# Optimization experiments

Measured on AMD Instinct MI355X. Metric: run time of the kernel, lower is better.

## Reference

```python
import jax, jax.numpy as jnp
import numpy as np

N_AGENTS = 8
N_ACTIONS = 14
STATE_DIM = 168
RNN_DIM = 64
GAT_DIM = 32
N_HEADS = 4
HYPER = 64


def setup_inputs() -> dict:
    key = jax.random.key(0)
    ks = jax.random.split(key, 16)
    bs, T = 256, 256
    def xavier(k, shape):
        fan_in, fan_out = shape[0], shape[-1]
        lim = float(np.sqrt(6.0 / (fan_in + fan_out)))
        return jax.random.uniform(k, shape, jnp.float32, -lim, lim)
    return {
        'agent_qs': jax.random.normal(ks[0], (bs, T, N_AGENTS), jnp.float32),
        'states': jax.random.normal(ks[1], (bs, T, STATE_DIM), jnp.float32),
        'max_q_i': jax.random.normal(ks[2], (bs, T, N_AGENTS), jnp.float32),
        'hidden_states': jax.random.normal(ks[3], (bs, T, N_AGENTS, RNN_DIM), jnp.float32),
        # hyper_w_final MLP
        'w1f': xavier(ks[4], (STATE_DIM, HYPER)), 'b1f': jnp.zeros((HYPER,), jnp.float32),
        'w2f': xavier(ks[5], (HYPER, N_AGENTS)), 'b2f': jnp.zeros((N_AGENTS,), jnp.float32),
        # V MLP
        'w1v': xavier(ks[6], (STATE_DIM, HYPER)), 'b1v': jnp.zeros((HYPER,), jnp.float32),
        'w2v': xavier(ks[7], (HYPER, N_AGENTS)), 'b2v': jnp.zeros((N_AGENTS,), jnp.float32),
        # GAT: W (no bias) and attention vector att_a [1, H, 2*d]
        'Wg': xavier(ks[8], (RNN_DIM, N_HEADS * GAT_DIM)),
        'att_a': xavier(ks[9], (1, N_HEADS, 2 * GAT_DIM)) * 1.414,
        # hyper_w_dvd linear
        'Wd': xavier(ks[10], (STATE_DIM, N_HEADS * GAT_DIM)), 'bd': jnp.zeros((N_HEADS * GAT_DIM,), jnp.float32),
    }


def reference(agent_qs, states, max_q_i, hidden_states,
              w1f, b1f, w2f, b2f, w1v, b1v, w2v, b2v,
              Wg, att_a, Wd, bd):
    bs = agent_qs.shape[0]
    S = states.reshape(-1, STATE_DIM)                     # [B, state_dim]
    q = agent_qs.reshape(-1, N_AGENTS)                    # [B, n]
    mq = max_q_i.reshape(-1, N_AGENTS)
    H = hidden_states.reshape(-1, N_AGENTS, RNN_DIM)      # [B, n, rnn]

    # weighted_head=True branch
    w_final = jnp.abs(jax.nn.relu(S @ w1f + b1f) @ w2f + b2f) + 1e-10
    v = jax.nn.relu(S @ w1v + b1v) @ w2v + b2v
    q = w_final * q + v
    mq = w_final * mq + v
    adv_q = jax.lax.stop_gradient(q - mq)                 # .detach() in torch

    # MultiHeadGAT on tiny agent graph, without materializing h_cat
    hp = jnp.einsum('bni,ihd->bhnd', H, Wg.reshape(RNN_DIM, N_HEADS, GAT_DIM))  # [B,h,n,d]
    a_i = att_a[0, :, :GAT_DIM]                           # [h, d]
    a_j = att_a[0, :, GAT_DIM:]
    e_i = jnp.einsum('bhnd,hd->bhn', hp, a_i)
    e_j = jnp.einsum('bhnd,hd->bhn', hp, a_j)
    e = e_i[:, :, :, None] + e_j[:, :, None, :]           # [B,h,n,n]
    e = jnp.where(e > 0, e, 0.2 * e)                      # LeakyReLU(0.2)
    attn = jax.nn.softmax(e, axis=-1)
    graphs = jax.nn.elu(jnp.einsum('bhij,bhjd->bhid', attn, hp))  # [B,h,n,d]

    # DVD weights
    w_dvd = (S @ Wd + bd).reshape(-1, N_HEADS, GAT_DIM)   # [B,h,d]
    weights_dvd = jnp.abs(jnp.einsum('bhd,bhnd->bhn', w_dvd, graphs))  # [B,h,n]
    adv_w_final = weights_dvd.mean(axis=1)                # [B,n]

    # is_minus_one=True
    adv_tot = jnp.sum(adv_q * (adv_w_final - 1.0), axis=1)
    return adv_tot.reshape(bs, -1, 1)
```

## Files before the change

### kernel.cpp

```cpp
#include <hip/hip_runtime.h>
#include <math.h>

#define STATE_DIM 168
#define BTOT 65536
#define SLS 1064

typedef float f32x4 __attribute__((ext_vector_type(4)));
typedef short bf16x8 __attribute__((ext_vector_type(8)));

union Frag { bf16x8 v; unsigned short u[8]; };
union Acc  { f32x4 v; float f[4]; };

__device__ __forceinline__ unsigned short f2bf(float f) {
    unsigned int u = __float_as_uint(f);
    u += 0x7fffu + ((u >> 16) & 1u);
    return (unsigned short)(u >> 16);
}

__global__ void __launch_bounds__(256, 5)
ffn_kernel(const float* __restrict__ states,
           const float* __restrict__ w1f, const float* __restrict__ b1f,
           const float* __restrict__ w2f, const float* __restrict__ b2f,
           const float* __restrict__ Wd,  const float* __restrict__ bd,
           float* __restrict__ wfin, float* __restrict__ wdvd)
{
    __shared__ float S_lds[4][8 * STATE_DIM];
    __shared__ float y1_lds[4][8 * 65];

    const int wid  = threadIdx.x >> 6;
    const int lane = threadIdx.x & 63;
    const int wgi  = blockIdx.x * 4 + wid;
    const long s0  = (long)wgi * 8;

    const float* Sg = states + s0 * STATE_DIM;
    float* Sl = S_lds[wid];
    #pragma unroll
    for (int i = 0; i < 21; ++i)
        Sl[lane + i * 64] = Sg[lane + i * 64];
    __syncthreads();

    float acc1[8], ad0[8], ad1[8];
    const float bb1  = b1f[lane];
    const float bdv0 = bd[lane];
    const float bdv1 = bd[lane + 64];
    #pragma unroll
    for (int s = 0; s < 8; ++s) { acc1[s] = bb1; ad0[s] = bdv0; ad1[s] = bdv1; }

    float w1c[4], wd0c[4], wd1c[4];
    #pragma unroll
    for (int kk = 0; kk < 4; ++kk) {
        w1c[kk]  = w1f[kk * 64 + lane];
        wd0c[kk] = Wd[kk * 128 + lane];
        wd1c[kk] = Wd[kk * 128 + 64 + lane];
    }

    for (int k = 0; k < STATE_DIM; k += 4) {
        const int kn = (k + 4 < STATE_DIM) ? (k + 4) : k;
        float w1n[4], wd0n[4], wd1n[4];
        #pragma unroll
        for (int kk = 0; kk < 4; ++kk) {
            w1n[kk]  = w1f[(kn + kk) * 64 + lane];
            wd0n[kk] = Wd[(kn + kk) * 128 + lane];
            wd1n[kk] = Wd[(kn + kk) * 128 + 64 + lane];
        }
        #pragma unroll
        for (int s = 0; s < 8; ++s) {
            const float4 sv = *(const float4*)&Sl[s * STATE_DIM + k];
            acc1[s] = fmaf(sv.x, w1c[0], acc1[s]);
            acc1[s] = fmaf(sv.y, w1c[1], acc1[s]);
            acc1[s] = fmaf(sv.z, w1c[2], acc1[s]);
            acc1[s] = fmaf(sv.w, w1c[3], acc1[s]);
            ad0[s] = fmaf(sv.x, wd0c[0], ad0[s]);
            ad0[s] = fmaf(sv.y, wd0c[1], ad0[s]);
            ad0[s] = fmaf(sv.z, wd0c[2], ad0[s]);
            ad0[s] = fmaf(sv.w, wd0c[3], ad0[s]);
            ad1[s] = fmaf(sv.x, wd1c[0], ad1[s]);
            ad1[s] = fmaf(sv.y, wd1c[1], ad1[s]);
            ad1[s] = fmaf(sv.z, wd1c[2], ad1[s]);
            ad1[s] = fmaf(sv.w, wd1c[3], ad1[s]);
        }
        #pragma unroll
        for (int kk = 0; kk < 4; ++kk) {
            w1c[kk] = w1n[kk]; wd0c[kk] = wd0n[kk]; wd1c[kk] = wd1n[kk];
        }
    }

    #pragma unroll
    for (int s = 0; s < 8; ++s) {
        y1_lds[wid][s * 65 + lane] = fmaxf(acc1[s], 0.0f);
        wdvd[(s0 + s) * 128 + lane]      = ad0[s];
        wdvd[(s0 + s) * 128 + 64 + lane] = ad1[s];
    }
    __syncthreads();

    {
        const int s = lane >> 3, n = lane & 7;
        float acc = b2f[n];
        #pragma unroll
        for (int j = 0; j < 64; ++j)
            acc = fmaf(y1_lds[wid][s * 65 + j], w2f[j * 8 + n], acc);
        wfin[(s0 + s) * 8 + n] = fabsf(acc) + 1e-10f;
    }
}

__global__ void __launch_bounds__(256, 3)
gat_kernel(const float* __restrict__ agent_qs,
           const float* __restrict__ max_q_i,
           const float* __restrict__ hidden,
           const float* __restrict__ Wg,
           const float* __restrict__ att_a,
           const float* __restrict__ wfin,
           const float* __restrict__ wdvd,
           float* __restrict__ out)
{
    __shared__ float hp_lds[4][2 * SLS];
    __shared__ float attn_lds[4][544];
    __shared__ float e_lds[4][128];
    __shared__ float ws_lds[4][64];
    __shared__ float a_lds[264];

    const int t    = threadIdx.x;
    const int wid  = t >> 6;
    const int lane = t & 63;

    {
        const int h = t >> 6, r = t & 63, wch = r >> 5, d = r & 31;
        a_lds[(h * 2 + wch) * 33 + d] = att_a[t];
    }
    __syncthreads();

    float* hp  = hp_lds[wid];
    float* at  = attn_lds[wid];
    float* el  = e_lds[wid];
    float* wsl = ws_lds[wid];

    const int wgid = blockIdx.x * 4 + wid;
    const int quad = lane >> 4;
    const int col  = lane & 15;

    Frag Bf[8][2];
    #pragma unroll
    for (int tt = 0; tt < 8; ++tt)
        #pragma unroll
        for (int ks = 0; ks < 2; ++ks)
            #pragma unroll
            for (int j = 0; j < 8; ++j)
                Bf[tt][ks].u[j] =
                    f2bf(Wg[(ks * 32 + quad * 8 + j) * 128 + tt * 16 + col]);

    const int sl_a = (lane >> 3) & 1;
    const int n_a  = lane & 7;
    const int sl_w = quad >> 1;
    const int nb   = (quad & 1) * 4;

    for (int g = 0; g < 4; ++g) {
        const long smp0 = (long)wgid * 8 + 2 * g;

        Frag A0, A1;
        {
            const float* Hb = hidden + (smp0 + sl_a) * 512 + n_a * 64 + quad * 8;
            const float4 h00 = *(const float4*)(Hb);
            const float4 h01 = *(const float4*)(Hb + 4);
            const float4 h10 = *(const float4*)(Hb + 32);
            const float4 h11 = *(const float4*)(Hb + 36);
            A0.u[0] = f2bf(h00.x); A0.u[1] = f2bf(h00.y);
            A0.u[2] = f2bf(h00.z); A0.u[3] = f2bf(h00.w);
            A0.u[4] = f2bf(h01.x); A0.u[5] = f2bf(h01.y);
            A0.u[6] = f2bf(h01.z); A0.u[7] = f2bf(h01.w);
            A1.u[0] = f2bf(h10.x); A1.u[1] = f2bf(h10.y);
            A1.u[2] = f2bf(h10.z); A1.u[3] = f2bf(h10.w);
            A1.u[4] = f2bf(h11.x); A1.u[5] = f2bf(h11.y);
            A1.u[6] = f2bf(h11.z); A1.u[7] = f2bf(h11.w);
        }

        #pragma unroll
        for (int tt = 0; tt < 8; ++tt) {
            Acc acc;
            acc.v = (f32x4){0.f, 0.f, 0.f, 0.f};
            acc.v = __builtin_amdgcn_mfma_f32_16x16x32_bf16(A0.v, Bf[tt][0].v, acc.v, 0, 0, 0);
            acc.v = __builtin_amdgcn_mfma_f32_16x16x32_bf16(A1.v, Bf[tt][1].v, acc.v, 0, 0, 0);
            const int c = tt * 16 + col;
            float4 st = {acc.f[0], acc.f[1], acc.f[2], acc.f[3]};
            *(float4*)&hp[sl_w * SLS + c * 8 + ((c >> 5) << 3) + nb] = st;
        }

        {
            const int h = lane >> 4, r = lane & 15, wch = r >> 3, n = r & 7;
            const float* arow = &a_lds[(h * 2 + wch) * 33];
            #pragma unroll
            for (int sl = 0; sl < 2; ++sl) {
                float acc = 0.f;
                #pragma unroll
                for (int d = 0; d < 32; ++d)
                    acc = fmaf(hp[sl * SLS + (h * 32 + d) * 8 + h * 8 + n],
                               arow[d], acc);
                el[sl * 64 + wch * 32 + h * 8 + n] = acc;
            }
        }

        {
            const int sl = lane >> 5, r = lane & 31, h = r >> 3, i = r & 7;
            const float eiv = el[sl * 64 + h * 8 + i];
            const float* ejp = &el[sl * 64 + 32 + h * 8];
            float e[8], mx = -1e30f;
            #pragma unroll
            for (int j = 0; j < 8; ++j) {
                float v = eiv + ejp[j];
                v = v > 0.f ? v : 0.2f * v;
                e[j] = v;
                mx = fmaxf(mx, v);
            }
            float ssum = 0.f;
            #pragma unroll
            for (int j = 0; j < 8; ++j) { e[j] = __expf(e[j] - mx); ssum += e[j]; }
            const float inv = 1.f / ssum;
            #pragma unroll
            for (int j = 0; j < 8; ++j)
                at[sl * 272 + h * 66 + i * 8 + j] = e[j] * inv;
        }

        {
            const int sl = lane >> 5, r = lane & 31, h = r >> 3, n = r & 7;
            const long smp = smp0 + sl;
            float ar[8];
            #pragma unroll
            for (int j = 0; j < 8; ++j)
                ar[j] = at[sl * 272 + h * 66 + n * 8 + j];
            float wdd[32];
            {
                const float* wdp = wdvd + smp * 128 + h * 32;
                #pragma unroll
                for (int q4 = 0; q4 < 8; ++q4) {
                    const float4 v = *(const float4*)(wdp + q4 * 4);
                    wdd[q4 * 4 + 0] = v.x; wdd[q4 * 4 + 1] = v.y;
                    wdd[q4 * 4 + 2] = v.z; wdd[q4 * 4 + 3] = v.w;
                }
            }
            float part = 0.f;
            #pragma unroll
            for (int d = 0; d < 32; ++d) {
                const int c = h * 32 + d;
                const float* hb = &hp[sl * SLS + c * 8 + h * 8];
                const float4 p0 = *(const float4*)(hb);
                const float4 p1 = *(const float4*)(hb + 4);
                float gg = ar[0] * p0.x;
                gg = fmaf(ar[1], p0.y, gg);
                gg = fmaf(ar[2], p0.z, gg);
                gg = fmaf(ar[3], p0.w, gg);
                gg = fmaf(ar[4], p1.x, gg);
                gg = fmaf(ar[5], p1.y, gg);
                gg = fmaf(ar[6], p1.z, gg);
                gg = fmaf(ar[7], p1.w, gg);
                gg = gg > 0.f ? gg : (__expf(gg) - 1.0f);
                part = fmaf(wdd[d], gg, part);
            }
            wsl[sl * 32 + h * 8 + n] = fabsf(part);
        }

        {
            const int sl = lane >> 5, r = lane & 31;
            if (r < 8) {
                const int n = r;
                const long smp = smp0 + sl;
                const float awf = 0.25f * (wsl[sl * 32 + n] + wsl[sl * 32 + 8 + n] +
                                           wsl[sl * 32 + 16 + n] + wsl[sl * 32 + 24 + n]);
                const float adv = wfin[smp * 8 + n] *
                                  (agent_qs[smp * 8 + n] - max_q_i[smp * 8 + n]);
                float p = adv * (awf - 1.0f);
                p += __shfl_xor(p, 4, 64);
                p += __shfl_xor(p, 2, 64);
                p += __shfl_xor(p, 1, 64);
                if (n == 0) out[smp] = p;
            }
        }
    }
}

extern "C" void kernel_launch(void* const* d_in, const int* in_sizes, int n_in,
                              void* d_out, int out_size, void* d_ws, size_t ws_size,
                              hipStream_t stream) {
    const float* agent_qs = (const float*)d_in[0];
    const float* states   = (const float*)d_in[1];
    const float* max_q_i  = (const float*)d_in[2];
    const float* hidden   = (const float*)d_in[3];
    const float* w1f = (const float*)d_in[4];
    const float* b1f = (const float*)d_in[5];
    const float* w2f = (const float*)d_in[6];
    const float* b2f = (const float*)d_in[7];
    const float* Wg    = (const float*)d_in[12];
    const float* att_a = (const float*)d_in[13];
    const float* Wd    = (const float*)d_in[14];
    const float* bd    = (const float*)d_in[15];
    float* out  = (float*)d_out;

    float* wfin = (float*)d_ws;
    float* wdvd = wfin + (size_t)BTOT * 8;

    ffn_kernel<<<2048, 256, 0, stream>>>(states, w1f, b1f, w2f, b2f, Wd, bd,
                                         wfin, wdvd);
    gat_kernel<<<2048, 256, 0, stream>>>(agent_qs, max_q_i, hidden, Wg, att_a,
                                         wfin, wdvd, out);
}
```

Measured before the change: 364.3 us.

## Rewrite state FFN kernel with bf16 MFMA and register-resident weight fragments

Replaces the scalar FP32 FMA loop of the FFN kernel with bf16 16x16x32 MFMA instructions. Weight fragments for w1f, Wd and w2f are converted to bf16 and held in registers once per block, while each block processes two 16-sample tiles staged through padded bf16 LDS. The intent is to cut the ALU cost of the 168-wide projections. It lowers precision to bf16 for the states and weights, and it leaves the separate GAT kernel unchanged.

```diff
diff --git a/kernel.cpp b/kernel.cpp
--- a/kernel.cpp
+++ b/kernel.cpp
@@ -4,6 +4,7 @@
 #define STATE_DIM 168
 #define BTOT 65536
 #define SLS 1064
+#define SPAD 184
 
 typedef float f32x4 __attribute__((ext_vector_type(4)));
 typedef short bf16x8 __attribute__((ext_vector_type(8)));
@@ -17,89 +18,116 @@
     return (unsigned short)(u >> 16);
 }
 
-__global__ void __launch_bounds__(256, 5)
+__global__ void __launch_bounds__(256)
 ffn_kernel(const float* __restrict__ states,
            const float* __restrict__ w1f, const float* __restrict__ b1f,
            const float* __restrict__ w2f, const float* __restrict__ b2f,
            const float* __restrict__ Wd,  const float* __restrict__ bd,
            float* __restrict__ wfin, float* __restrict__ wdvd)
 {
-    __shared__ float S_lds[4][8 * STATE_DIM];
-    __shared__ float y1_lds[4][8 * 65];
-
-    const int wid  = threadIdx.x >> 6;
-    const int lane = threadIdx.x & 63;
-    const int wgi  = blockIdx.x * 4 + wid;
-    const long s0  = (long)wgi * 8;
-
-    const float* Sg = states + s0 * STATE_DIM;
-    float* Sl = S_lds[wid];
+    __shared__ unsigned short S_bf[16 * SPAD];
+    __shared__ float y1[16 * 72];
+
+    const int t    = threadIdx.x;
+    const int wid  = t >> 6;
+    const int lane = t & 63;
+    const int quad = lane >> 4;
+    const int col  = lane & 15;
+
+    Frag B[3][6];
     #pragma unroll
-    for (int i = 0; i < 21; ++i)
-        Sl[lane + i * 64] = Sg[lane + i * 64];
-    __syncthreads();
-
-    float acc1[8], ad0[8], ad1[8];
-    const float bb1  = b1f[lane];
-    const float bdv0 = bd[lane];
-    const float bdv1 = bd[lane + 64];
+    for (int ks = 0; ks < 6; ++ks)
+        #pragma unroll
+        for (int j = 0; j < 8; ++j) {
+            const int k = ks * 32 + quad * 8 + j;
+            const bool v = (k < STATE_DIM);
+            B[0][ks].u[j] = v ? f2bf(w1f[k * 64 + wid * 16 + col]) : (unsigned short)0;
+            B[1][ks].u[j] = v ? f2bf(Wd[k * 128 + wid * 32 + col]) : (unsigned short)0;
+            B[2][ks].u[j] = v ? f2bf(Wd[k * 128 + wid * 32 + 16 + col]) : (unsigned short)0;
+        }
+    Frag B2[2];
     #pragma unroll
-    for (int s = 0; s < 8; ++s) { acc1[s] = bb1; ad0[s] = bdv0; ad1[s] = bdv1; }
-
-    float w1c[4], wd0c[4], wd1c[4];
-    #pragma unroll
-    for (int kk = 0; kk < 4; ++kk) {
-        w1c[kk]  = w1f[kk * 64 + lane];
-        wd0c[kk] = Wd[kk * 128 + lane];
-        wd1c[kk] = Wd[kk * 128 + 64 + lane];
-    }
-
-    for (int k = 0; k < STATE_DIM; k += 4) {
-        const int kn = (k + 4 < STATE_DIM) ? (k + 4) : k;
-        float w1n[4], wd0n[4], wd1n[4];
-        #pragma unroll
-        for (int kk = 0; kk < 4; ++kk) {
-            w1n[kk]  = w1f[(kn + kk) * 64 + lane];
-            wd0n[kk] = Wd[(kn + kk) * 128 + lane];
-            wd1n[kk] = Wd[(kn + kk) * 128 + 64 + lane];
-        }
-        #pragma unroll
-        for (int s = 0; s < 8; ++s) {
-            const float4 sv = *(const float4*)&Sl[s * STATE_DIM + k];
-            acc1[s] = fmaf(sv.x, w1c[0], acc1[s]);
-            acc1[s] = fmaf(sv.y, w1c[1], acc1[s]);
-            acc1[s] = fmaf(sv.z, w1c[2], acc1[s]);
-            acc1[s] = fmaf(sv.w, w1c[3], acc1[s]);
-            ad0[s] = fmaf(sv.x, wd0c[0], ad0[s]);
-            ad0[s] = fmaf(sv.y, wd0c[1], ad0[s]);
-            ad0[s] = fmaf(sv.z, wd0c[2], ad0[s]);
-            ad0[s] = fmaf(sv.w, wd0c[3], ad0[s]);
-            ad1[s] = fmaf(sv.x, wd1c[0], ad1[s]);
-            ad1[s] = fmaf(sv.y, wd1c[1], ad1[s]);
-            ad1[s] = fmaf(sv.z, wd1c[2], ad1[s]);
-            ad1[s] = fmaf(sv.w, wd1c[3], ad1[s]);
-        }
-        #pragma unroll
-        for (int kk = 0; kk < 4; ++kk) {
-            w1c[kk] = w1n[kk]; wd0c[kk] = wd0n[kk]; wd1c[kk] = wd1n[kk];
-        }
-    }
-
-    #pragma unroll
-    for (int s = 0; s < 8; ++s) {
-        y1_lds[wid][s * 65 + lane] = fmaxf(acc1[s], 0.0f);
-        wdvd[(s0 + s) * 128 + lane]      = ad0[s];
-        wdvd[(s0 + s) * 128 + 64 + lane] = ad1[s];
-    }
-    __syncthreads();
-
-    {
-        const int s = lane >> 3, n = lane & 7;
-        float acc = b2f[n];
-        #pragma unroll
-        for (int j = 0; j < 64; ++j)
-            acc = fmaf(y1_lds[wid][s * 65 + j], w2f[j * 8 + n], acc);
-        wfin[(s0 + s) * 8 + n] = fabsf(acc) + 1e-10f;
+    for (int ks = 0; ks < 2; ++ks)
+        #pragma unroll
+        for (int j = 0; j < 8; ++j) {
+            const int k = ks * 32 + quad * 8 + j;
+            B2[ks].u[j] = (col < 8) ? f2bf(w2f[k * 8 + col]) : (unsigned short)0;
+        }
+
+    const float bias1  = b1f[wid * 16 + col];
+    const float biasd0 = bd[wid * 32 + col];
+    const float biasd1 = bd[wid * 32 + 16 + col];
+    const float bias2  = (col < 8) ? b2f[col] : 0.0f;
+
+    for (int it = 0; it < 2; ++it) {
+        const long smp0 = ((long)blockIdx.x * 2 + it) * 16;
+
+        {
+            const int r = t >> 4, u = t & 15;
+            const float* Srow = states + (smp0 + r) * STATE_DIM;
+            #pragma unroll
+            for (int i = 0; i < 12; ++i) {
+                const int k = u + 16 * i;
+                if (k < SPAD) {
+                    unsigned short vv = (k < STATE_DIM) ? f2bf(Srow[k])
+                                                        : (unsigned short)0;
+                    S_bf[r * SPAD + k] = vv;
+                }
+            }
+        }
+        __syncthreads();
+
+        Frag A[6];
+        #pragma unroll
+        for (int ks = 0; ks < 6; ++ks) {
+            int k0 = ks * 32 + quad * 8;
+            if (ks == 5 && quad != 0) k0 = STATE_DIM;
+            A[ks].v = *(const bf16x8*)&S_bf[col * SPAD + k0];
+        }
+
+        Acc D0, D1, D2t;
+        D0.v = (f32x4){0.f,0.f,0.f,0.f};
+        D1.v = (f32x4){0.f,0.f,0.f,0.f};
+        D2t.v = (f32x4){0.f,0.f,0.f,0.f};
+        #pragma unroll
+        for (int ks = 0; ks < 6; ++ks) {
+            D0.v  = __builtin_amdgcn_mfma_f32_16x16x32_bf16(A[ks].v, B[0][ks].v, D0.v, 0, 0, 0);
+            D1.v  = __builtin_amdgcn_mfma_f32_16x16x32_bf16(A[ks].v, B[1][ks].v, D1.v, 0, 0, 0);
+            D2t.v = __builtin_amdgcn_mfma_f32_16x16x32_bf16(A[ks].v, B[2][ks].v, D2t.v, 0, 0, 0);
+        }
+
+        #pragma unroll
+        for (int r = 0; r < 4; ++r) {
+            const int m = quad * 4 + r;
+            y1[m * 72 + wid * 16 + col] = fmaxf(D0.f[r] + bias1, 0.0f);
+            wdvd[(smp0 + m) * 128 + wid * 32 + col]      = D1.f[r]  + biasd0;
+            wdvd[(smp0 + m) * 128 + wid * 32 + 16 + col] = D2t.f[r] + biasd1;
+        }
+        __syncthreads();
+
+        {
+            Frag A2[2];
+            #pragma unroll
+            for (int ks = 0; ks < 2; ++ks) {
+                const float4 p0 = *(const float4*)&y1[col * 72 + ks * 32 + quad * 8];
+                const float4 p1 = *(const float4*)&y1[col * 72 + ks * 32 + quad * 8 + 4];
+                A2[ks].u[0] = f2bf(p0.x); A2[ks].u[1] = f2bf(p0.y);
+                A2[ks].u[2] = f2bf(p0.z); A2[ks].u[3] = f2bf(p0.w);
+                A2[ks].u[4] = f2bf(p1.x); A2[ks].u[5] = f2bf(p1.y);
+                A2[ks].u[6] = f2bf(p1.z); A2[ks].u[7] = f2bf(p1.w);
+            }
+            Acc Dw;
+            Dw.v = (f32x4){0.f,0.f,0.f,0.f};
+            Dw.v = __builtin_amdgcn_mfma_f32_16x16x32_bf16(A2[0].v, B2[0].v, Dw.v, 0, 0, 0);
+            Dw.v = __builtin_amdgcn_mfma_f32_16x16x32_bf16(A2[1].v, B2[1].v, Dw.v, 0, 0, 0);
+            if (wid == 0 && col < 8) {
+                #pragma unroll
+                for (int r = 0; r < 4; ++r)
+                    wfin[(smp0 + quad * 4 + r) * 8 + col] =
+                        fabsf(Dw.f[r] + bias2) + 1e-10f;
+            }
+        }
+        __syncthreads();
     }
 }
 
```

After: 331.3 us. 1.1x faster.
